# Kernel optimization log

Hardware: AMD Instinct MI355X
Metric: run time of the kernel (lower is better)

The kernel has to match this reference:

```python
import jax, jax.numpy as jnp
import numpy as np

BSZ, MAXQ, DH = 64, 32, 300
N_ENT, N_REL, N_TRI = 100000, 18, 600000
NUM_STEPS = 3
D_CLS = 1024


def setup_inputs() -> dict:
    key = jax.random.key(0)
    ks = jax.random.split(key, 20)
    s = 1.0 / np.sqrt(DH)
    inp = {
        "q_word_h": jax.random.normal(ks[0], (BSZ, MAXQ, DH), jnp.float32),
        "q_embeddings": jax.random.normal(ks[1], (BSZ, DH), jnp.float32),
        "e_s": jax.random.uniform(ks[2], (BSZ, N_ENT), jnp.float32),
        # per-step encoders: Linear(300,300)+Tanh, stacked over steps
        "W_step": jax.random.normal(ks[3], (NUM_STEPS, DH, DH), jnp.float32) * s,
        "b_step": jnp.zeros((NUM_STEPS, DH), jnp.float32),
        "W_cq": jax.random.normal(ks[4], (2 * DH, DH), jnp.float32) * s,
        "b_cq": jnp.zeros((DH,), jnp.float32),
        "W_ca": jax.random.normal(ks[5], (DH,), jnp.float32) * s,
        "b_ca": jnp.zeros((), jnp.float32),
        "W_rel": jax.random.normal(ks[6], (DH, N_REL), jnp.float32) * s,
        "b_rel": jnp.zeros((N_REL,), jnp.float32),
        "ent_emb": jax.random.normal(ks[7], (N_ENT, DH), jnp.float32) * s,
        "W_e1": jax.random.normal(ks[8], (DH, D_CLS), jnp.float32) * s,
        "b_e1": jnp.zeros((D_CLS,), jnp.float32),
        "W_e2": jax.random.normal(ks[9], (D_CLS, N_ENT), jnp.float32) / np.sqrt(D_CLS),
        "b_e2": jnp.zeros((N_ENT,), jnp.float32),
        # sparse KG triple lists (Msubj/Mrel/Mobj one-hot selectors)
        "subj_idx": jax.random.randint(ks[10], (N_TRI,), 0, N_ENT, jnp.int32),
        "rel_idx": jax.random.randint(ks[11], (N_TRI,), 0, N_REL, jnp.int32),
        "obj_idx": jax.random.randint(ks[12], (N_TRI,), 0, N_ENT, jnp.int32),
    }
    return inp


def _follow(e, r, subj_idx, rel_idx, obj_idx):
    # x[t, b] = e[b, subj[t]] * r[b, rel[t]];  out[b, o] = sum_{t: obj[t]=o} x[t, b]
    x = jnp.take(e, subj_idx, axis=1) * jnp.take(r, rel_idx, axis=1)  # [bsz, n_tri]
    return jax.ops.segment_sum(x.T, obj_idx, num_segments=N_ENT).T    # [bsz, n_ent]


def reference(q_word_h, q_embeddings, e_s, W_step, b_step, W_cq, b_cq, W_ca, b_ca,
              W_rel, b_rel, ent_emb, W_e1, b_e1, W_e2, b_e2,
              subj_idx, rel_idx, obj_idx):
    last_e = e_s
    last_c = jnp.zeros((q_word_h.shape[0], DH), q_word_h.dtype)
    for t in range(NUM_STEPS):
        q_t = jnp.tanh(q_embeddings @ W_step[t] + b_step[t])                 # [b, d]
        cq_t = jnp.concatenate([last_c, q_t], axis=1) @ W_cq + b_cq          # [b, d]
        # ca_linear((cq_t[:,None,:] * q_word_h)) -> logits over words
        q_logits = jnp.einsum('bd,bqd,d->bq', cq_t, q_word_h, W_ca) + b_ca   # [b, q]
        q_dist = jax.nn.softmax(q_logits, axis=1)
        last_c = jnp.einsum('bq,bqd->bd', q_dist, q_word_h)                  # attended ctx
        rel_dist = jax.nn.softmax(last_c @ W_rel + b_rel, axis=1)            # [b, n_rel]
        last_e = _follow(last_e, rel_dist, subj_idx, rel_idx, obj_idx)       # [b, n_ent]
    normed = last_e / (jnp.sum(last_e, axis=1, keepdims=True) + 1e-6)
    pred_e = normed @ ent_emb                                                # [b, d]
    pred_e = jnp.maximum(pred_e @ W_e1 + b_e1, 0.0) @ W_e2 + b_e2            # [b, n_ent]
    return pred_e
```

## Files before the change

### kernel.cpp

```cpp
#include <hip/hip_runtime.h>
#include <cstdint>
#include <utility>

#define BSZ   64
#define MAXQ  32
#define DH    300
#define N_ENT 100000
#define N_REL 18
#define N_TRI 600000
#define D_CLS 1024

__global__ __launch_bounds__(256) void k_transpose(const float* __restrict__ e_s,
                                                   float* __restrict__ e_t) {
  __shared__ float T[64][65];
  int e0 = blockIdx.x * 64;
  int lane = threadIdx.x & 63;
  int w = threadIdx.x >> 6;
  for (int b = w; b < 64; b += 4) {
    int e = e0 + lane;
    T[b][lane] = (e < N_ENT) ? e_s[b * N_ENT + e] : 0.f;
  }
  __syncthreads();
  for (int i = w; i < 64; i += 4) {
    int e = e0 + i;
    if (e < N_ENT) e_t[e * 64 + lane] = T[lane][i];
  }
}

__global__ __launch_bounds__(320) void k_step(
    const float* __restrict__ qwh, const float* __restrict__ qemb,
    const float* __restrict__ Wstep, const float* __restrict__ bstep,
    const float* __restrict__ Wcq, const float* __restrict__ bcq,
    const float* __restrict__ Wca, const float* __restrict__ bca,
    const float* __restrict__ Wrel, const float* __restrict__ brel,
    float* __restrict__ last_c, float* __restrict__ rel_dist, int t) {
  int b = blockIdx.x;
  int tid = threadIdx.x;
  __shared__ float qe[DH], qtL[DH], lcL[DH], wcq[DH];
  __shared__ float lg[MAXQ], red[MAXQ * 8], dist[MAXQ];
  __shared__ float relL[N_REL];
  __shared__ float mx, sm;

  for (int j = tid; j < DH; j += 320) {
    qe[j] = qemb[b * DH + j];
    lcL[j] = last_c[b * DH + j];
  }
  __syncthreads();

  const float* Wt = Wstep + t * DH * DH;
  for (int j = tid; j < DH; j += 320) {
    float acc = bstep[t * DH + j];
    for (int k = 0; k < DH; k++) acc += qe[k] * Wt[k * DH + j];
    qtL[j] = tanhf(acc);
  }
  __syncthreads();

  for (int j = tid; j < DH; j += 320) {
    float acc = bcq[j];
    for (int k = 0; k < DH; k++) acc += lcL[k] * Wcq[k * DH + j];
    for (int k = 0; k < DH; k++) acc += qtL[k] * Wcq[(DH + k) * DH + j];
    wcq[j] = acc * Wca[j];
  }
  __syncthreads();

  if (tid < MAXQ * 8) {
    int q = tid >> 3, sub = tid & 7;
    const float* row = qwh + (b * MAXQ + q) * DH;
    float acc = 0.f;
    for (int d = sub; d < DH; d += 8) acc += wcq[d] * row[d];
    red[tid] = acc;
  }
  __syncthreads();
  if (tid < MAXQ) {
    float acc = bca[0];
    for (int s = 0; s < 8; s++) acc += red[tid * 8 + s];
    lg[tid] = acc;
  }
  __syncthreads();
  if (tid == 0) {
    float m = lg[0];
    for (int q = 1; q < MAXQ; q++) m = fmaxf(m, lg[q]);
    mx = m;
  }
  __syncthreads();
  if (tid < MAXQ) dist[tid] = expf(lg[tid] - mx);
  __syncthreads();
  if (tid == 0) {
    float s = 0.f;
    for (int q = 0; q < MAXQ; q++) s += dist[q];
    sm = s;
  }
  __syncthreads();

  for (int j = tid; j < DH; j += 320) {
    float acc = 0.f;
    for (int q = 0; q < MAXQ; q++) acc += dist[q] * qwh[(b * MAXQ + q) * DH + j];
    acc /= sm;
    lcL[j] = acc;
    last_c[b * DH + j] = acc;
  }
  __syncthreads();

  if (tid < N_REL) {
    float acc = brel[tid];
    for (int d = 0; d < DH; d++) acc += lcL[d] * Wrel[d * N_REL + tid];
    relL[tid] = acc;
  }
  __syncthreads();
  if (tid == 0) {
    float m = relL[0];
    for (int r = 1; r < N_REL; r++) m = fmaxf(m, relL[r]);
    mx = m;
  }
  __syncthreads();
  if (tid < N_REL) relL[tid] = expf(relL[tid] - mx);
  __syncthreads();
  if (tid == 0) {
    float s = 0.f;
    for (int r = 0; r < N_REL; r++) s += relL[r];
    sm = s;
  }
  __syncthreads();
  if (tid < N_REL) rel_dist[b * N_REL + tid] = relL[tid] / sm;
}

__global__ __launch_bounds__(256) void k_follow(
    const float* __restrict__ e_in, const float* __restrict__ rel_dist,
    const int* __restrict__ subj, const int* __restrict__ rel,
    const int* __restrict__ obj, float* __restrict__ e_out) {
  __shared__ float relL[BSZ * N_REL];
  for (int i = threadIdx.x; i < BSZ * N_REL; i += 256) relL[i] = rel_dist[i];
  __syncthreads();
  int lane = threadIdx.x & 63;
  int wave = (blockIdx.x << 2) | (threadIdx.x >> 6);
  int nwaves = gridDim.x << 2;
  for (int i = wave; i < N_TRI; i += nwaves) {
    int s = subj[i], r = rel[i], o = obj[i];
    float x = e_in[s * 64 + lane] * relL[lane * N_REL + r];
    atomicAdd(&e_out[o * 64 + lane], x);
  }
}

__global__ __launch_bounds__(256) void k_sums(const float* __restrict__ e,
                                              float* __restrict__ sums) {
  __shared__ float red[4][64];
  int lane = threadIdx.x & 63;
  int w = threadIdx.x >> 6;
  int gw = blockIdx.x * 4 + w;
  int nw = gridDim.x * 4;
  float acc = 0.f;
  for (int ent = gw; ent < N_ENT; ent += nw) acc += e[ent * 64 + lane];
  red[w][lane] = acc;
  __syncthreads();
  if (threadIdx.x < 64) {
    float s = red[0][threadIdx.x] + red[1][threadIdx.x] +
              red[2][threadIdx.x] + red[3][threadIdx.x];
    atomicAdd(&sums[threadIdx.x], s);
  }
}

#define PF_NB 400
#define PF_EPB 250
#define PF_CH 32
#define PF_RS 304
__global__ __launch_bounds__(256) void k_predfeat(
    const float* __restrict__ e, const float* __restrict__ sums,
    const float* __restrict__ ent_emb, float* __restrict__ partials) {
  __shared__ float embL[PF_CH * PF_RS];
  __shared__ float eL[PF_CH * 64];
  int tid = threadIdx.x;
  int b = tid & 63, g = tid >> 6;
  int e0 = blockIdx.x * PF_EPB;
  int e1 = e0 + PF_EPB;

  int sb = (4 * tid) & 63;
  float4 inv4 = make_float4(1.f / (sums[sb + 0] + 1e-6f), 1.f / (sums[sb + 1] + 1e-6f),
                            1.f / (sums[sb + 2] + 1e-6f), 1.f / (sums[sb + 3] + 1e-6f));

  float4 acc[19];
  #pragma unroll
  for (int k = 0; k < 19; k++) acc[k] = make_float4(0.f, 0.f, 0.f, 0.f);

  float4* embL4 = (float4*)embL;
  float4* eL4 = (float4*)eL;

  for (int ecur = e0; ecur < e1; ecur += PF_CH) {
    int n = min(PF_CH, e1 - ecur);
    __syncthreads();
    const float4* src = (const float4*)(ent_emb + (size_t)ecur * DH);
    for (int i = tid; i < n * 75; i += 256) {
      int ee = i / 75, j = i - ee * 75;
      embL4[ee * 76 + j] = src[i];
      if (j == 0) embL4[ee * 76 + 75] = make_float4(0.f, 0.f, 0.f, 0.f);
    }
    const float4* esrc = (const float4*)(e + (size_t)ecur * 64);
    for (int i = tid; i < n * 16; i += 256) {
      float4 v = esrc[i];
      v.x *= inv4.x; v.y *= inv4.y; v.z *= inv4.z; v.w *= inv4.w;
      eL4[i] = v;
    }
    __syncthreads();
    for (int ee = 0; ee < n; ee++) {
      float ev = eL[ee * 64 + b];
      const float4* em = embL4 + ee * 76 + g * 19;
      #pragma unroll
      for (int k = 0; k < 19; k++) {
        float4 m = em[k];
        acc[k].x += ev * m.x;
        acc[k].y += ev * m.y;
        acc[k].z += ev * m.z;
        acc[k].w += ev * m.w;
      }
    }
  }

  float* pout = partials + (size_t)blockIdx.x * (PF_RS * 64);
  #pragma unroll
  for (int k = 0; k < 19; k++) {
    int d = g * 76 + k * 4;
    pout[(d + 0) * 64 + b] = acc[k].x;
    pout[(d + 1) * 64 + b] = acc[k].y;
    pout[(d + 2) * 64 + b] = acc[k].z;
    pout[(d + 3) * 64 + b] = acc[k].w;
  }
}

__global__ __launch_bounds__(256) void k_reduce_pf(const float* __restrict__ partials,
                                                   float* __restrict__ pf) {
  int j = blockIdx.x * 256 + threadIdx.x;
  if (j >= DH * 64) return;
  int d = j >> 6, b = j & 63;
  float acc = 0.f;
  for (int c = 0; c < PF_NB; c++) acc += partials[(size_t)c * (PF_RS * 64) + j];
  pf[b * DH + d] = acc;
}

__global__ __launch_bounds__(256) void k_hidden(const float* __restrict__ pf,
                                                const float* __restrict__ We1,
                                                const float* __restrict__ be1,
                                                float* __restrict__ hiddenT) {
  int idx = blockIdx.x * 256 + threadIdx.x;
  int j = idx & (D_CLS - 1);
  int b = idx >> 10;
  float acc = be1[j];
  const float* p = pf + b * DH;
  for (int k = 0; k < DH; k++) acc += p[k] * We1[k * D_CLS + j];
  hiddenT[j * 64 + b] = fmaxf(acc, 0.f);
}

__global__ __launch_bounds__(256) void k_init_out(const float* __restrict__ be2,
                                                  float* __restrict__ out) {
  int idx4 = blockIdx.x * 256 + threadIdx.x;
  int elem = idx4 * 4;
  if (elem >= BSZ * N_ENT) return;
  int o = elem % N_ENT;
  float4 bv = *(const float4*)(be2 + o);
  ((float4*)out)[idx4] = bv;
}

#define KF_SPLIT 4
#define KF_KC (D_CLS / KF_SPLIT)
__global__ __launch_bounds__(256) void k_final(const float* __restrict__ hT,
                                               const float* __restrict__ We2,
                                               float* __restrict__ out) {
  int tid = threadIdx.x;
  int o = blockIdx.x * 256 + tid;
  bool valid = (o < N_ENT);
  int oc = valid ? o : 0;
  int k0 = blockIdx.y * KF_KC;

  float acc[64];
  #pragma unroll
  for (int b = 0; b < 64; b++) acc[b] = 0.f;

  const float* h = hT + (size_t)k0 * 64;
  const float* w = We2 + (size_t)k0 * N_ENT + oc;
  #pragma unroll 2
  for (int k = 0; k < KF_KC; k++) {
    float wv = w[(size_t)k * N_ENT];
    const float* hk = h + k * 64;
    #pragma unroll
    for (int b = 0; b < 64; b++) acc[b] += hk[b] * wv;
  }

  if (valid) {
    #pragma unroll
    for (int b = 0; b < 64; b++)
      atomicAdd(&out[(size_t)b * N_ENT + o], acc[b]);
  }
}

extern "C" void kernel_launch(void* const* d_in, const int* in_sizes, int n_in,
                              void* d_out, int out_size, void* d_ws, size_t ws_size,
                              hipStream_t stream) {
  const float* qwh   = (const float*)d_in[0];
  const float* qemb  = (const float*)d_in[1];
  const float* e_s   = (const float*)d_in[2];
  const float* Wstep = (const float*)d_in[3];
  const float* bstep = (const float*)d_in[4];
  const float* Wcq   = (const float*)d_in[5];
  const float* bcq   = (const float*)d_in[6];
  const float* Wca   = (const float*)d_in[7];
  const float* bca   = (const float*)d_in[8];
  const float* Wrel  = (const float*)d_in[9];
  const float* brel  = (const float*)d_in[10];
  const float* eemb  = (const float*)d_in[11];
  const float* We1   = (const float*)d_in[12];
  const float* be1   = (const float*)d_in[13];
  const float* We2   = (const float*)d_in[14];
  const float* be2   = (const float*)d_in[15];
  const int* subj    = (const int*)d_in[16];
  const int* rel     = (const int*)d_in[17];
  const int* obj     = (const int*)d_in[18];
  float* out = (float*)d_out;

  float* ws = (float*)d_ws;
  float* e_a      = ws;
  float* e_b      = e_a + (size_t)N_ENT * 64;
  float* last_c   = e_b + (size_t)N_ENT * 64;
  float* rel_d    = last_c + BSZ * DH;
  float* sums     = rel_d + BSZ * N_REL;
  float* pf       = sums + 64;
  float* hiddenT  = pf + BSZ * DH;
  float* partials = hiddenT + BSZ * D_CLS;

  hipMemsetAsync(last_c, 0, (size_t)(BSZ * DH + BSZ * N_REL + 64) * sizeof(float), stream);

  k_transpose<<<(N_ENT + 63) / 64, 256, 0, stream>>>(e_s, e_a);

  float* cur = e_a;
  float* nxt = e_b;
  for (int t = 0; t < 3; t++) {
    k_step<<<BSZ, 320, 0, stream>>>(qwh, qemb, Wstep, bstep, Wcq, bcq, Wca, bca,
                                    Wrel, brel, last_c, rel_d, t);
    hipMemsetAsync(nxt, 0, (size_t)N_ENT * 64 * sizeof(float), stream);
    k_follow<<<2048, 256, 0, stream>>>(cur, rel_d, subj, rel, obj, nxt);
    std::swap(cur, nxt);
  }

  k_sums<<<256, 256, 0, stream>>>(cur, sums);
  k_predfeat<<<PF_NB, 256, 0, stream>>>(cur, sums, eemb, partials);
  k_reduce_pf<<<(DH * 64 + 255) / 256, 256, 0, stream>>>(partials, pf);
  k_hidden<<<(BSZ * D_CLS) / 256, 256, 0, stream>>>(pf, We1, be1, hiddenT);
  k_init_out<<<(BSZ * N_ENT / 4 + 255) / 256, 256, 0, stream>>>(be2, out);
  dim3 fgrid((N_ENT + 255) / 256, KF_SPLIT);
  k_final<<<fgrid, 256, 0, stream>>>(hiddenT, We2, out);
}
```

Before: 1.586 ms.

## Fuse sums into follow, drop atomics in final GEMM, batch memsets

The entity-sum reduction moves into the last follow kernel: each wave accumulates its contributions and adds them atomically to the per-batch sums. The final GEMM now tiles over batch groups instead of splitting K, writes bias plus result directly without atomics, and drops the init kernel. The per-step memsets become one memset over three distinct buffers. The predfeat grid is retuned to 512 blocks, and partials reuse a spent buffer. The final GEMM now reads We2 four times (once per batch group) in exchange for removing the atomics and the init pass.

```diff
diff --git a/kernel.cpp b/kernel.cpp
--- a/kernel.cpp
+++ b/kernel.cpp
@@ -1,6 +1,5 @@
 #include <hip/hip_runtime.h>
 #include <cstdint>
-#include <utility>
 
 #define BSZ   64
 #define MAXQ  32
@@ -127,40 +126,26 @@
 __global__ __launch_bounds__(256) void k_follow(
     const float* __restrict__ e_in, const float* __restrict__ rel_dist,
     const int* __restrict__ subj, const int* __restrict__ rel,
-    const int* __restrict__ obj, float* __restrict__ e_out) {
+    const int* __restrict__ obj, float* __restrict__ e_out,
+    float* __restrict__ sums) {
   __shared__ float relL[BSZ * N_REL];
   for (int i = threadIdx.x; i < BSZ * N_REL; i += 256) relL[i] = rel_dist[i];
   __syncthreads();
   int lane = threadIdx.x & 63;
   int wave = (blockIdx.x << 2) | (threadIdx.x >> 6);
   int nwaves = gridDim.x << 2;
+  float sacc = 0.f;
   for (int i = wave; i < N_TRI; i += nwaves) {
     int s = subj[i], r = rel[i], o = obj[i];
     float x = e_in[s * 64 + lane] * relL[lane * N_REL + r];
+    sacc += x;
     atomicAdd(&e_out[o * 64 + lane], x);
   }
-}
-
-__global__ __launch_bounds__(256) void k_sums(const float* __restrict__ e,
-                                              float* __restrict__ sums) {
-  __shared__ float red[4][64];
-  int lane = threadIdx.x & 63;
-  int w = threadIdx.x >> 6;
-  int gw = blockIdx.x * 4 + w;
-  int nw = gridDim.x * 4;
-  float acc = 0.f;
-  for (int ent = gw; ent < N_ENT; ent += nw) acc += e[ent * 64 + lane];
-  red[w][lane] = acc;
-  __syncthreads();
-  if (threadIdx.x < 64) {
-    float s = red[0][threadIdx.x] + red[1][threadIdx.x] +
-              red[2][threadIdx.x] + red[3][threadIdx.x];
-    atomicAdd(&sums[threadIdx.x], s);
-  }
-}
-
-#define PF_NB 400
-#define PF_EPB 250
+  if (sums) atomicAdd(&sums[lane], sacc);
+}
+
+#define PF_NB 512
+#define PF_EPB 196
 #define PF_CH 32
 #define PF_RS 304
 __global__ __launch_bounds__(256) void k_predfeat(
@@ -172,6 +157,7 @@
   int b = tid & 63, g = tid >> 6;
   int e0 = blockIdx.x * PF_EPB;
   int e1 = e0 + PF_EPB;
+  if (e1 > N_ENT) e1 = N_ENT;
 
   int sb = (4 * tid) & 63;
   float4 inv4 = make_float4(1.f / (sums[sb + 0] + 1e-6f), 1.f / (sums[sb + 1] + 1e-6f),
@@ -248,45 +234,41 @@
   hiddenT[j * 64 + b] = fmaxf(acc, 0.f);
 }
 
-__global__ __launch_bounds__(256) void k_init_out(const float* __restrict__ be2,
-                                                  float* __restrict__ out) {
-  int idx4 = blockIdx.x * 256 + threadIdx.x;
-  int elem = idx4 * 4;
-  if (elem >= BSZ * N_ENT) return;
-  int o = elem % N_ENT;
-  float4 bv = *(const float4*)(be2 + o);
-  ((float4*)out)[idx4] = bv;
-}
-
-#define KF_SPLIT 4
-#define KF_KC (D_CLS / KF_SPLIT)
+#define FO_TILE 512
 __global__ __launch_bounds__(256) void k_final(const float* __restrict__ hT,
                                                const float* __restrict__ We2,
+                                               const float* __restrict__ be2,
                                                float* __restrict__ out) {
   int tid = threadIdx.x;
-  int o = blockIdx.x * 256 + tid;
-  bool valid = (o < N_ENT);
-  int oc = valid ? o : 0;
-  int k0 = blockIdx.y * KF_KC;
-
-  float acc[64];
+  int o0 = blockIdx.x * FO_TILE + tid * 2;
+  int bg = blockIdx.y * 16;
+  bool valid = (o0 < N_ENT);
+  int oc = valid ? o0 : 0;
+
+  float2 acc[16];
   #pragma unroll
-  for (int b = 0; b < 64; b++) acc[b] = 0.f;
-
-  const float* h = hT + (size_t)k0 * 64;
-  const float* w = We2 + (size_t)k0 * N_ENT + oc;
-  #pragma unroll 2
-  for (int k = 0; k < KF_KC; k++) {
-    float wv = w[(size_t)k * N_ENT];
+  for (int i = 0; i < 16; i++) acc[i] = make_float2(0.f, 0.f);
+
+  const float* h = hT + bg;
+  const float* w = We2 + oc;
+  #pragma unroll 4
+  for (int k = 0; k < D_CLS; k++) {
+    float2 wv = *(const float2*)(w + (size_t)k * N_ENT);
     const float* hk = h + k * 64;
     #pragma unroll
-    for (int b = 0; b < 64; b++) acc[b] += hk[b] * wv;
+    for (int i = 0; i < 16; i++) {
+      acc[i].x += hk[i] * wv.x;
+      acc[i].y += hk[i] * wv.y;
+    }
   }
 
   if (valid) {
+    float2 bv = *(const float2*)(be2 + oc);
     #pragma unroll
-    for (int b = 0; b < 64; b++)
-      atomicAdd(&out[(size_t)b * N_ENT + o], acc[b]);
+    for (int i = 0; i < 16; i++) {
+      float2 v = make_float2(acc[i].x + bv.x, acc[i].y + bv.y);
+      *(float2*)(out + (size_t)(bg + i) * N_ENT + o0) = v;
+    }
   }
 }
 
@@ -315,34 +297,34 @@
   float* out = (float*)d_out;
 
   float* ws = (float*)d_ws;
-  float* e_a      = ws;
-  float* e_b      = e_a + (size_t)N_ENT * 64;
-  float* last_c   = e_b + (size_t)N_ENT * 64;
-  float* rel_d    = last_c + BSZ * DH;
-  float* sums     = rel_d + BSZ * N_REL;
-  float* pf       = sums + 64;
-  float* hiddenT  = pf + BSZ * DH;
-  float* partials = hiddenT + BSZ * D_CLS;
-
-  hipMemsetAsync(last_c, 0, (size_t)(BSZ * DH + BSZ * N_REL + 64) * sizeof(float), stream);
-
-  k_transpose<<<(N_ENT + 63) / 64, 256, 0, stream>>>(e_s, e_a);
-
-  float* cur = e_a;
-  float* nxt = e_b;
+  const size_t EB = (size_t)N_ENT * 64;
+  float* eb0     = ws;
+  float* eb1     = ws + EB;
+  float* eb2     = ws + 2 * EB;
+  float* eb3     = ws + 3 * EB;
+  float* last_c  = ws + 4 * EB;
+  float* sums    = last_c + BSZ * DH;
+  float* rel_d   = sums + 64;
+  float* pf      = rel_d + BSZ * N_REL;
+  float* hiddenT = pf + BSZ * DH;
+  float* partials = eb1;
+
+  hipMemsetAsync(last_c, 0, (size_t)(BSZ * DH + 64) * sizeof(float), stream);
+  hipMemsetAsync(eb1, 0, 3 * EB * sizeof(float), stream);
+
+  k_transpose<<<(N_ENT + 63) / 64, 256, 0, stream>>>(e_s, eb0);
+
+  float* chain[4] = {eb0, eb1, eb2, eb3};
   for (int t = 0; t < 3; t++) {
     k_step<<<BSZ, 320, 0, stream>>>(qwh, qemb, Wstep, bstep, Wcq, bcq, Wca, bca,
                                     Wrel, brel, last_c, rel_d, t);
-    hipMemsetAsync(nxt, 0, (size_t)N_ENT * 64 * sizeof(float), stream);
-    k_follow<<<2048, 256, 0, stream>>>(cur, rel_d, subj, rel, obj, nxt);
-    std::swap(cur, nxt);
-  }
-
-  k_sums<<<256, 256, 0, stream>>>(cur, sums);
-  k_predfeat<<<PF_NB, 256, 0, stream>>>(cur, sums, eemb, partials);
+    k_follow<<<2048, 256, 0, stream>>>(chain[t], rel_d, subj, rel, obj, chain[t + 1],
+                                       (t == 2) ? sums : nullptr);
+  }
+
+  k_predfeat<<<PF_NB, 256, 0, stream>>>(eb3, sums, eemb, partials);
   k_reduce_pf<<<(DH * 64 + 255) / 256, 256, 0, stream>>>(partials, pf);
   k_hidden<<<(BSZ * D_CLS) / 256, 256, 0, stream>>>(pf, We1, be1, hiddenT);
-  k_init_out<<<(BSZ * N_ENT / 4 + 255) / 256, 256, 0, stream>>>(be2, out);
-  dim3 fgrid((N_ENT + 255) / 256, KF_SPLIT);
-  k_final<<<fgrid, 256, 0, stream>>>(hiddenT, We2, out);
-}
+  dim3 fgrid((N_ENT + FO_TILE - 1) / FO_TILE, 4);
+  k_final<<<fgrid, 256, 0, stream>>>(hiddenT, We2, be2, out);
+}
```

After: 1.730 ms. 1.09x slower.
